# Kernel optimization log

Measured on AMD Instinct MI355X. Metric: run time of the kernel, lower is better.

## Reference

```python
import jax, jax.numpy as jnp
import numpy as np

N = 300000
H = 700
W_GRID = 700
CIN = 64
COUT = 64
K = 9


def setup_inputs() -> dict:
    rng = np.random.default_rng(0)
    lin = rng.permutation(H * W_GRID)[:N]
    ys = (lin // W_GRID).astype(np.int64)
    xs = (lin % W_GRID).astype(np.int64)
    grid = np.full(H * W_GRID, -1, np.int32)
    grid[lin] = np.arange(N, dtype=np.int32)
    offs = [(dy, dx) for dy in (-1, 0, 1) for dx in (-1, 0, 1)]

    def build(d):
        nbr = np.full((K, N), -1, np.int32)
        for k, (dy, dx) in enumerate(offs):
            ny = ys + dy * d
            nx = xs + dx * d
            valid = (ny >= 0) & (ny < H) & (nx >= 0) & (nx < W_GRID)
            l = np.clip(ny * W_GRID + nx, 0, H * W_GRID - 1)
            nbr[k] = np.where(valid, grid[l], -1)
        return jnp.asarray(nbr)

    nbr_d1 = build(1)
    nbr_d2 = build(2)

    key = jax.random.key(0)
    ks = jax.random.split(key, 16)
    f32 = jnp.float32

    def bn(k, c):
        s = jax.random.uniform(k, (c,), f32, 0.5, 1.5)
        b = jax.random.normal(jax.random.fold_in(k, 1), (c,), f32) * 0.1
        return s, b

    features = jax.random.normal(ks[0], (N, CIN), f32)
    W1 = jax.random.normal(ks[1], (K, CIN, COUT), f32) * 0.05
    W2a = jax.random.normal(ks[2], (CIN, COUT // 2), f32) * 0.05
    W2b = jax.random.normal(ks[3], (K, COUT // 2, COUT), f32) * 0.05
    W3 = jax.random.normal(ks[4], (K, CIN, COUT), f32) * 0.05
    Wf = jax.random.normal(ks[5], (3 * COUT, COUT), f32) * 0.05
    A1_w = jax.random.normal(ks[6], (3 * COUT, COUT // 4), f32) * 0.1
    A1_b = jnp.zeros((COUT // 4,), f32)
    A2_w = jax.random.normal(ks[7], (COUT // 4, 3 * COUT), f32) * 0.1
    A2_b = jnp.zeros((3 * COUT,), f32)
    bn1_s, bn1_b = bn(ks[8], COUT)
    bn2a_s, bn2a_b = bn(ks[9], COUT // 2)
    bn2b_s, bn2b_b = bn(ks[10], COUT)
    bn3_s, bn3_b = bn(ks[11], COUT)
    bnf_s, bnf_b = bn(ks[12], COUT)

    return dict(features=features, W1=W1, bn1_s=bn1_s, bn1_b=bn1_b,
                W2a=W2a, bn2a_s=bn2a_s, bn2a_b=bn2a_b,
                W2b=W2b, bn2b_s=bn2b_s, bn2b_b=bn2b_b,
                W3=W3, bn3_s=bn3_s, bn3_b=bn3_b,
                A1_w=A1_w, A1_b=A1_b, A2_w=A2_w, A2_b=A2_b,
                Wf=Wf, bnf_s=bnf_s, bnf_b=bnf_b,
                nbr_d1=nbr_d1, nbr_d2=nbr_d2)


def _sconv(f, nbr, W):
    # f: [N, Cin], nbr: [K, N] (-1 = no neighbor), W: [K, Cin, Cout]
    mask = (nbr >= 0)[..., None]                      # [K, N, 1]
    g = jnp.where(mask, f[jnp.clip(nbr, 0)], 0.0)     # [K, N, Cin] gather
    return jnp.einsum('knc,kcd->nd', g, W)            # [N, Cout]


def _bnrelu(x, s, b):
    # inference-mode BatchNorm folded into affine scale/shift, then ReLU
    return jax.nn.relu(x * s + b)


def reference(features, W1, bn1_s, bn1_b, W2a, bn2a_s, bn2a_b, W2b, bn2b_s, bn2b_b,
              W3, bn3_s, bn3_b, A1_w, A1_b, A2_w, A2_b, Wf, bnf_s, bnf_b,
              nbr_d1, nbr_d2):
    # path 1: 3x3 sparse conv + BN + ReLU
    feat1 = _bnrelu(_sconv(features, nbr_d1, W1), bn1_s, bn1_b)
    # path 2: 1x1 bottleneck + 3x3 sparse conv
    h = _bnrelu(features @ W2a, bn2a_s, bn2a_b)
    feat2 = _bnrelu(_sconv(h, nbr_d1, W2b), bn2b_s, bn2b_b)
    # path 3: 3x3 dilated (d=2) sparse conv
    feat3 = _bnrelu(_sconv(features, nbr_d2, W3), bn3_s, bn3_b)
    ms = jnp.concatenate([feat1, feat2, feat3], axis=1)   # [N, 3*Cout]
    # SE-style attention from global max pool over active sites
    pooled = jnp.max(ms, axis=0)                          # [3*Cout]
    attn = jax.nn.sigmoid(jax.nn.relu(pooled @ A1_w + A1_b) @ A2_w + A2_b)
    ms = ms * attn
    # 1x1 fusion conv + BN + ReLU
    fused = _bnrelu(ms @ Wf, bnf_s, bnf_b)                # [N, Cout]
    return fused
```

## Files before the change

### kernel.cpp

```cpp
#include <hip/hip_runtime.h>

#define N_PTS 300000
#define NPAD  300032
#define ZROW  N_PTS

typedef _Float16 f16;
typedef _Float16 f16x8 __attribute__((ext_vector_type(8)));
typedef float    f32x4 __attribute__((ext_vector_type(4)));

__device__ __forceinline__ f16 f2h(float x) { return (f16)x; }

union u4f16 { uint4 u; f16x8 h; };

#define HEAD_BLOCKS (NPAD / 256)
#define WP_BLOCKS   360


__global__ __launch_bounds__(256) void k_head(
    const float* __restrict__ feat, const float* __restrict__ W2a,
    const float* __restrict__ s2a, const float* __restrict__ b2a,
    const float* __restrict__ W1, const float* __restrict__ W2b,
    const float* __restrict__ W3,
    f16* __restrict__ featf, f16* __restrict__ hf,
    f16* __restrict__ Wt1, f16* __restrict__ Wt2b, f16* __restrict__ Wt3)
{
    if (blockIdx.x >= HEAD_BLOCKS) {
        int i = (blockIdx.x - HEAD_BLOCKS) * 256 + threadIdx.x;
        if (i < 36864) {
            int j = i & 7, lane = (i >> 3) & 63, nt = (i >> 9) & 3,
                ks = (i >> 11) & 1, k = i >> 12;
            int d = ks * 32 + (lane >> 4) * 8 + j, c = nt * 16 + (lane & 15);
            Wt1[i] = f2h(W1[(k << 12) + (d << 6) + c]);
        } else if (i < 73728) {
            int ii = i - 36864;
            int j = ii & 7, lane = (ii >> 3) & 63, nt = (ii >> 9) & 3,
                ks = (ii >> 11) & 1, k = ii >> 12;
            int d = ks * 32 + (lane >> 4) * 8 + j, c = nt * 16 + (lane & 15);
            Wt3[ii] = f2h(W3[(k << 12) + (d << 6) + c]);
        } else if (i < 92160) {
            int ii = i - 73728;
            int j = ii & 7, lane = (ii >> 3) & 63, nt = (ii >> 9) & 3, k = ii >> 11;
            int d = (lane >> 4) * 8 + j, c = nt * 16 + (lane & 15);
            Wt2b[ii] = f2h(W2b[k * 2048 + (d << 6) + c]);
        }
        return;
    }

    int lane = threadIdx.x & 63, wave = threadIdx.x >> 6;
    int n0 = (blockIdx.x * 4 + wave) * 64;
    int ln = lane & 15, q = lane >> 4;

    f16x8 a[4][2];
#pragma unroll
    for (int mt = 0; mt < 4; mt++) {
        int n = n0 + mt * 16 + ln;
#pragma unroll
        for (int ks = 0; ks < 2; ks++) {
            u4f16 v;
            if (n < N_PTS) {
                const float* p = feat + (long)n * 64 + ks * 32 + q * 8;
                float4 lo = *(const float4*)p;
                float4 hi = *(const float4*)(p + 4);
                v.h[0] = f2h(lo.x); v.h[1] = f2h(lo.y);
                v.h[2] = f2h(lo.z); v.h[3] = f2h(lo.w);
                v.h[4] = f2h(hi.x); v.h[5] = f2h(hi.y);
                v.h[6] = f2h(hi.z); v.h[7] = f2h(hi.w);
            } else {
                v.u = make_uint4(0u, 0u, 0u, 0u);
            }
            a[mt][ks] = v.h;
            *(uint4*)(featf + (long)n * 64 + ks * 32 + q * 8) = v.u;
        }
    }

    f32x4 acc[4][2];
    for (int mt = 0; mt < 4; mt++) for (int nt = 0; nt < 2; nt++)
        acc[mt][nt] = (f32x4){0.f, 0.f, 0.f, 0.f};
#pragma unroll
    for (int ks = 0; ks < 2; ks++)
#pragma unroll
        for (int nt = 0; nt < 2; nt++) {
            f16x8 b;
#pragma unroll
            for (int j = 0; j < 8; j++)
                b[j] = f2h(W2a[(ks * 32 + q * 8 + j) * 32 + nt * 16 + ln]);
#pragma unroll
            for (int mt = 0; mt < 4; mt++)
                acc[mt][nt] = __builtin_amdgcn_mfma_f32_16x16x32_f16(a[mt][ks], b, acc[mt][nt], 0, 0, 0);
        }

#pragma unroll
    for (int nt = 0; nt < 2; nt++) {
        int ch = nt * 16 + ln;
        float s = s2a[ch], bb = b2a[ch];
#pragma unroll
        for (int mt = 0; mt < 4; mt++)
#pragma unroll
            for (int r = 0; r < 4; r++) {
                int n = n0 + mt * 16 + q * 4 + r;
                float v = (n < N_PTS) ? fmaxf(acc[mt][nt][r] * s + bb, 0.f) : 0.f;
                hf[(long)n * 32 + ch] = f2h(v);
            }
    }
}

template <int CIN>
__device__ __forceinline__ void loadrows(
    uint4 (&dst)[4][CIN / 32], const int (&idx)[4],
    const f16* __restrict__ src, int q)
{
#pragma unroll
    for (int mt = 0; mt < 4; mt++) {
        const f16* p = src + (long)idx[mt] * CIN + q * 8;
#pragma unroll
        for (int ks = 0; ks < CIN / 32; ks++)
            dst[mt][ks] = *(const uint4*)(p + ks * 32);
    }
}

__device__ __forceinline__ void loadidx(
    int (&dst)[4], const int* __restrict__ nbr, int k, int n0, int ln)
{
    const int* nb = nbr + k * N_PTS;
#pragma unroll
    for (int mt = 0; mt < 4; mt++) {
        int nn = n0 + mt * 16 + ln;
        int v = (nn < N_PTS) ? nb[nn] : -1;
        dst[mt] = (v < 0) ? ZROW : v;
    }
}

template <int CIN>
__device__ __forceinline__ void conv_path(
    const f16* __restrict__ src, const f16* WtL,
    const int* __restrict__ nbr,
    int lane, int n0,
    const float* __restrict__ bns, const float* __restrict__ bnb,
    f16* __restrict__ msf, int colBase, float* __restrict__ pooled)
{
    constexpr int KS = CIN / 32;
    int ln = lane & 15, q = lane >> 4;

    f32x4 acc[4][4];
    for (int mt = 0; mt < 4; mt++) for (int nt = 0; nt < 4; nt++)
        acc[mt][nt] = (f32x4){0.f, 0.f, 0.f, 0.f};

    int  idxr[4][4];
    uint4 raw[4][4][KS];

#pragma unroll
    for (int k = 0; k < 4; k++) loadidx(idxr[k], nbr, k, n0, ln);
#pragma unroll
    for (int k = 0; k < 3; k++) loadrows<CIN>(raw[k], idxr[k], src, q);
    __builtin_amdgcn_sched_barrier(0);

#pragma unroll
    for (int k = 0; k < 9; k++) {
        if (k + 3 < 9) loadrows<CIN>(raw[(k + 3) & 3], idxr[(k + 3) & 3], src, q);
        if (k + 4 < 9) loadidx(idxr[k & 3], nbr, k + 4, n0, ln);
        __builtin_amdgcn_sched_barrier(0);
        const f16* Wk = WtL + k * (KS * 4 * 512);
        __builtin_amdgcn_s_setprio(1);
#pragma unroll
        for (int ks = 0; ks < KS; ks++)
#pragma unroll
            for (int nt = 0; nt < 4; nt++) {
                f16x8 b = *(const f16x8*)(Wk + (ks * 4 + nt) * 512 + lane * 8);
#pragma unroll
                for (int mt = 0; mt < 4; mt++) {
                    u4f16 v; v.u = raw[k & 3][mt][ks];
                    acc[mt][nt] = __builtin_amdgcn_mfma_f32_16x16x32_f16(v.h, b, acc[mt][nt], 0, 0, 0);
                }
            }
        __builtin_amdgcn_s_setprio(0);
    }

#pragma unroll
    for (int nt = 0; nt < 4; nt++) {
        int ch = colBase + nt * 16 + ln;
        float s = bns[nt * 16 + ln], bb = bnb[nt * 16 + ln];
        float cmax = 0.f;
#pragma unroll
        for (int mt = 0; mt < 4; mt++)
#pragma unroll
            for (int r = 0; r < 4; r++) {
                int n = n0 + mt * 16 + q * 4 + r;
                float v = fmaxf(acc[mt][nt][r] * s + bb, 0.f);
                msf[(long)n * 192 + ch] = f2h(v);
                if (n < N_PTS) cmax = fmaxf(cmax, v);
            }
        cmax = fmaxf(cmax, __shfl_xor(cmax, 16));
        cmax = fmaxf(cmax, __shfl_xor(cmax, 32));
        if (q == 0) atomicMax((int*)(pooled + ch), __float_as_int(cmax));
    }
}

__global__ __launch_bounds__(512, 2) void k_conv(
    const f16* __restrict__ featf, const f16* __restrict__ hf,
    const f16* __restrict__ Wt1, const f16* __restrict__ Wt2b, const f16* __restrict__ Wt3,
    const int* __restrict__ nbr1, const int* __restrict__ nbr2,
    const float* __restrict__ bn1_s, const float* __restrict__ bn1_b,
    const float* __restrict__ bn2b_s, const float* __restrict__ bn2b_b,
    const float* __restrict__ bn3_s, const float* __restrict__ bn3_b,
    f16* __restrict__ msf, float* __restrict__ pooled)
{
    __shared__ f16 smem[9 * 64 * 64];

    int path = blockIdx.x % 3;
    int g    = blockIdx.x / 3;
    int lane = threadIdx.x & 63, wave = threadIdx.x >> 6;
    int n0 = (g * 8 + wave) * 64;

    const f16* Wsrc = (path == 0) ? Wt1 : (path == 1) ? Wt2b : Wt3;
    int nchunk = (path == 1) ? (9 * 32 * 64 / 8) : (9 * 64 * 64 / 8);
    for (int i = threadIdx.x; i < nchunk; i += 512)
        ((uint4*)smem)[i] = ((const uint4*)Wsrc)[i];
    __syncthreads();

    if (path == 0)
        conv_path<64>(featf, smem, nbr1, lane, n0, bn1_s,  bn1_b,  msf, 0,   pooled);
    else if (path == 1)
        conv_path<32>(hf,    smem, nbr1, lane, n0, bn2b_s, bn2b_b, msf, 64,  pooled);
    else
        conv_path<64>(featf, smem, nbr2, lane, n0, bn3_s,  bn3_b,  msf, 128, pooled);
}

__global__ __launch_bounds__(256) void k_attn(
    const float* __restrict__ pooled,
    const float* __restrict__ A1w, const float* __restrict__ A1b,
    const float* __restrict__ A2w, const float* __restrict__ A2b,
    const float* __restrict__ Wf, f16* __restrict__ Wfst)
{
    __shared__ float sp[192], sa1[16], sattn[192];
    int t = threadIdx.x;
    if (t < 192) sp[t] = pooled[t];
    __syncthreads();
    if (t < 16) {
        float acc = A1b[t];
        for (int i = 0; i < 192; i++) acc += sp[i] * A1w[i * 16 + t];
        sa1[t] = fmaxf(acc, 0.f);
    }
    __syncthreads();
    if (t < 192) {
        float acc = A2b[t];
        for (int i = 0; i < 16; i++) acc += sa1[i] * A2w[i * 192 + t];
        sattn[t] = 1.f / (1.f + expf(-acc));
    }
    __syncthreads();
    for (int i = t; i < 12288; i += 256) {
        int j = i & 7, lane = (i >> 3) & 63, nt = (i >> 9) & 3, kt = i >> 11;
        int jrow = kt * 32 + (lane >> 4) * 8 + j, c = nt * 16 + (lane & 15);
        Wfst[i] = f2h(Wf[jrow * 64 + c] * sattn[jrow]);
    }
}

__global__ __launch_bounds__(256, 4) void k_fuse(
    const f16* __restrict__ msf, const f16* __restrict__ Wfst,
    const float* __restrict__ sf, const float* __restrict__ bf_,
    float* __restrict__ out)
{
    int lane = threadIdx.x & 63, wave = threadIdx.x >> 6;
    int n0 = (blockIdx.x * 4 + wave) * 32;
    int ln = lane & 15, q = lane >> 4;

    uint4 araw[6][2];
#pragma unroll
    for (int kt = 0; kt < 6; kt++)
#pragma unroll
        for (int mt = 0; mt < 2; mt++)
            araw[kt][mt] = *(const uint4*)(msf + (long)(n0 + mt * 16 + ln) * 192 + kt * 32 + q * 8);

    f32x4 acc[2][4];
    for (int mt = 0; mt < 2; mt++) for (int nt = 0; nt < 4; nt++)
        acc[mt][nt] = (f32x4){0.f, 0.f, 0.f, 0.f};

#pragma unroll
    for (int kt = 0; kt < 6; kt++)
#pragma unroll
        for (int nt = 0; nt < 4; nt++) {
            f16x8 b = *(const f16x8*)(Wfst + ((kt * 4 + nt) * 64 + lane) * 8);
#pragma unroll
            for (int mt = 0; mt < 2; mt++) {
                u4f16 v; v.u = araw[kt][mt];
                acc[mt][nt] = __builtin_amdgcn_mfma_f32_16x16x32_f16(v.h, b, acc[mt][nt], 0, 0, 0);
            }
        }

#pragma unroll
    for (int nt = 0; nt < 4; nt++) {
        int ch = nt * 16 + ln;
        float s = sf[ch], bb = bf_[ch];
#pragma unroll
        for (int mt = 0; mt < 2; mt++)
#pragma unroll
            for (int r = 0; r < 4; r++) {
                int n = n0 + mt * 16 + q * 4 + r;
                if (n < N_PTS)
                    out[(long)n * 64 + ch] = fmaxf(acc[mt][nt][r] * s + bb, 0.f);
            }
    }
}

extern "C" void kernel_launch(void* const* d_in, const int* in_sizes, int n_in,
                              void* d_out, int out_size, void* d_ws, size_t ws_size,
                              hipStream_t stream)
{
    const float* features = (const float*)d_in[0];
    const float* W1     = (const float*)d_in[1];
    const float* bn1_s  = (const float*)d_in[2];
    const float* bn1_b  = (const float*)d_in[3];
    const float* W2a    = (const float*)d_in[4];
    const float* bn2a_s = (const float*)d_in[5];
    const float* bn2a_b = (const float*)d_in[6];
    const float* W2b    = (const float*)d_in[7];
    const float* bn2b_s = (const float*)d_in[8];
    const float* bn2b_b = (const float*)d_in[9];
    const float* W3     = (const float*)d_in[10];
    const float* bn3_s  = (const float*)d_in[11];
    const float* bn3_b  = (const float*)d_in[12];
    const float* A1w    = (const float*)d_in[13];
    const float* A1b    = (const float*)d_in[14];
    const float* A2w    = (const float*)d_in[15];
    const float* A2b    = (const float*)d_in[16];
    const float* Wf     = (const float*)d_in[17];
    const float* bnf_s  = (const float*)d_in[18];
    const float* bnf_b  = (const float*)d_in[19];
    const int*   nbr1   = (const int*)d_in[20];
    const int*   nbr2   = (const int*)d_in[21];

    char* ws = (char*)d_ws;
    size_t off = 0;
    f16* featf = (f16*)(ws + off); off += (size_t)NPAD * 64 * 2;
    f16* hf    = (f16*)(ws + off); off += (size_t)NPAD * 32 * 2;
    f16* msf   = (f16*)(ws + off); off += (size_t)NPAD * 192 * 2;
    f16* Wt1   = (f16*)(ws + off); off += 9 * 64 * 64 * 2;
    f16* Wt3   = (f16*)(ws + off); off += 9 * 64 * 64 * 2;
    f16* Wt2b  = (f16*)(ws + off); off += 9 * 32 * 64 * 2;
    f16* Wfst  = (f16*)(ws + off); off += 192 * 64 * 2;
    float* pooled = (float*)(ws + off); off += 256 * 4;

    hipMemsetAsync(pooled, 0, 192 * sizeof(float), stream);

    k_head<<<HEAD_BLOCKS + WP_BLOCKS, 256, 0, stream>>>(
        features, W2a, bn2a_s, bn2a_b, W1, W2b, W3,
        featf, hf, Wt1, Wt2b, Wt3);
    k_conv<<<(NPAD / 64 / 8) * 3, 512, 0, stream>>>(featf, hf, Wt1, Wt2b, Wt3, nbr1, nbr2,
                                           bn1_s, bn1_b, bn2b_s, bn2b_b, bn3_s, bn3_b,
                                           msf, pooled);
    k_attn<<<1, 256, 0, stream>>>(pooled, A1w, A1b, A2w, A2b, Wf, Wfst);
    k_fuse<<<NPAD / 128, 256, 0, stream>>>(msf, Wfst, bnf_s, bnf_b, (float*)d_out);
}
```

Before: 419.6 us.

## Fuse attention into fusion kernel, halve conv weight LDS, use nontemporal stores

Removes the separate single-block attention kernel by having every fusion block recompute the SE attention and the attention-scaled fused weights into shared memory. The conv kernel now stages weights in two phases (first 4 taps, then 5) with an LDS footprint of 5 slices instead of 9, adding extra barriers mid-loop. Intermediate and output stores and the msf loads use nontemporal hints. The per-block recomputation of attention and weight transform adds redundant work to every fusion block in exchange for one fewer launch and dependency.

```diff
diff --git a/kernel.cpp b/kernel.cpp
--- a/kernel.cpp
+++ b/kernel.cpp
@@ -7,10 +7,11 @@
 typedef _Float16 f16;
 typedef _Float16 f16x8 __attribute__((ext_vector_type(8)));
 typedef float    f32x4 __attribute__((ext_vector_type(4)));
+typedef unsigned int u32x4 __attribute__((ext_vector_type(4)));
 
 __device__ __forceinline__ f16 f2h(float x) { return (f16)x; }
 
-union u4f16 { uint4 u; f16x8 h; };
+union u4f16 { uint4 u; u32x4 v; f16x8 h; };
 
 #define HEAD_BLOCKS (NPAD / 256)
 #define WP_BLOCKS   360
@@ -132,14 +133,19 @@
 
 template <int CIN>
 __device__ __forceinline__ void conv_path(
-    const f16* __restrict__ src, const f16* WtL,
+    const f16* __restrict__ src, f16* smem, const f16* __restrict__ Wsrc,
     const int* __restrict__ nbr,
-    int lane, int n0,
+    int lane, int n0, int tid,
     const float* __restrict__ bns, const float* __restrict__ bnb,
     f16* __restrict__ msf, int colBase, float* __restrict__ pooled)
 {
     constexpr int KS = CIN / 32;
+    constexpr int SLICE = CIN * 64;
     int ln = lane & 15, q = lane >> 4;
+
+    for (int i = tid; i < 4 * SLICE / 8; i += 512)
+        ((uint4*)smem)[i] = ((const uint4*)Wsrc)[i];
+    __syncthreads();
 
     f32x4 acc[4][4];
     for (int mt = 0; mt < 4; mt++) for (int nt = 0; nt < 4; nt++)
@@ -156,10 +162,16 @@
 
 #pragma unroll
     for (int k = 0; k < 9; k++) {
+        if (k == 4) {
+            __syncthreads();
+            for (int i = tid; i < 5 * SLICE / 8; i += 512)
+                ((uint4*)smem)[i] = ((const uint4*)(Wsrc + 4 * SLICE))[i];
+            __syncthreads();
+        }
         if (k + 3 < 9) loadrows<CIN>(raw[(k + 3) & 3], idxr[(k + 3) & 3], src, q);
         if (k + 4 < 9) loadidx(idxr[k & 3], nbr, k + 4, n0, ln);
         __builtin_amdgcn_sched_barrier(0);
-        const f16* Wk = WtL + k * (KS * 4 * 512);
+        const f16* Wk = smem + (k < 4 ? k : k - 4) * SLICE;
         __builtin_amdgcn_s_setprio(1);
 #pragma unroll
         for (int ks = 0; ks < KS; ks++)
@@ -186,7 +198,7 @@
             for (int r = 0; r < 4; r++) {
                 int n = n0 + mt * 16 + q * 4 + r;
                 float v = fmaxf(acc[mt][nt][r] * s + bb, 0.f);
-                msf[(long)n * 192 + ch] = f2h(v);
+                __builtin_nontemporal_store(f2h(v), &msf[(long)n * 192 + ch]);
                 if (n < N_PTS) cmax = fmaxf(cmax, v);
             }
         cmax = fmaxf(cmax, __shfl_xor(cmax, 16));
@@ -204,71 +216,65 @@
     const float* __restrict__ bn3_s, const float* __restrict__ bn3_b,
     f16* __restrict__ msf, float* __restrict__ pooled)
 {
-    __shared__ f16 smem[9 * 64 * 64];
+    __shared__ f16 smem[5 * 64 * 64];
 
     int path = blockIdx.x % 3;
     int g    = blockIdx.x / 3;
     int lane = threadIdx.x & 63, wave = threadIdx.x >> 6;
     int n0 = (g * 8 + wave) * 64;
-
-    const f16* Wsrc = (path == 0) ? Wt1 : (path == 1) ? Wt2b : Wt3;
-    int nchunk = (path == 1) ? (9 * 32 * 64 / 8) : (9 * 64 * 64 / 8);
-    for (int i = threadIdx.x; i < nchunk; i += 512)
-        ((uint4*)smem)[i] = ((const uint4*)Wsrc)[i];
-    __syncthreads();
+    int tid = threadIdx.x;
 
     if (path == 0)
-        conv_path<64>(featf, smem, nbr1, lane, n0, bn1_s,  bn1_b,  msf, 0,   pooled);
+        conv_path<64>(featf, smem, Wt1,  nbr1, lane, n0, tid, bn1_s,  bn1_b,  msf, 0,   pooled);
     else if (path == 1)
-        conv_path<32>(hf,    smem, nbr1, lane, n0, bn2b_s, bn2b_b, msf, 64,  pooled);
+        conv_path<32>(hf,    smem, Wt2b, nbr1, lane, n0, tid, bn2b_s, bn2b_b, msf, 64,  pooled);
     else
-        conv_path<64>(featf, smem, nbr2, lane, n0, bn3_s,  bn3_b,  msf, 128, pooled);
-}
-
-__global__ __launch_bounds__(256) void k_attn(
-    const float* __restrict__ pooled,
+        conv_path<64>(featf, smem, Wt3,  nbr2, lane, n0, tid, bn3_s,  bn3_b,  msf, 128, pooled);
+}
+
+__global__ __launch_bounds__(256, 4) void k_fuse(
+    const f16* __restrict__ msf, const float* __restrict__ pooled,
     const float* __restrict__ A1w, const float* __restrict__ A1b,
     const float* __restrict__ A2w, const float* __restrict__ A2b,
-    const float* __restrict__ Wf, f16* __restrict__ Wfst)
+    const float* __restrict__ Wf,
+    const float* __restrict__ sf, const float* __restrict__ bf_,
+    float* __restrict__ out)
 {
     __shared__ float sp[192], sa1[16], sattn[192];
+    __shared__ f16 sWf[12288];
     int t = threadIdx.x;
     if (t < 192) sp[t] = pooled[t];
     __syncthreads();
     if (t < 16) {
-        float acc = A1b[t];
-        for (int i = 0; i < 192; i++) acc += sp[i] * A1w[i * 16 + t];
-        sa1[t] = fmaxf(acc, 0.f);
+        float a = A1b[t];
+        for (int i = 0; i < 192; i++) a += sp[i] * A1w[i * 16 + t];
+        sa1[t] = fmaxf(a, 0.f);
     }
     __syncthreads();
     if (t < 192) {
-        float acc = A2b[t];
-        for (int i = 0; i < 16; i++) acc += sa1[i] * A2w[i * 192 + t];
-        sattn[t] = 1.f / (1.f + expf(-acc));
+        float a = A2b[t];
+        for (int i = 0; i < 16; i++) a += sa1[i] * A2w[i * 192 + t];
+        sattn[t] = 1.f / (1.f + expf(-a));
     }
     __syncthreads();
     for (int i = t; i < 12288; i += 256) {
         int j = i & 7, lane = (i >> 3) & 63, nt = (i >> 9) & 3, kt = i >> 11;
         int jrow = kt * 32 + (lane >> 4) * 8 + j, c = nt * 16 + (lane & 15);
-        Wfst[i] = f2h(Wf[jrow * 64 + c] * sattn[jrow]);
-    }
-}
-
-__global__ __launch_bounds__(256, 4) void k_fuse(
-    const f16* __restrict__ msf, const f16* __restrict__ Wfst,
-    const float* __restrict__ sf, const float* __restrict__ bf_,
-    float* __restrict__ out)
-{
+        sWf[i] = f2h(Wf[jrow * 64 + c] * sattn[jrow]);
+    }
+    __syncthreads();
+
     int lane = threadIdx.x & 63, wave = threadIdx.x >> 6;
     int n0 = (blockIdx.x * 4 + wave) * 32;
     int ln = lane & 15, q = lane >> 4;
 
-    uint4 araw[6][2];
+    u32x4 araw[6][2];
 #pragma unroll
     for (int kt = 0; kt < 6; kt++)
 #pragma unroll
         for (int mt = 0; mt < 2; mt++)
-            araw[kt][mt] = *(const uint4*)(msf + (long)(n0 + mt * 16 + ln) * 192 + kt * 32 + q * 8);
+            araw[kt][mt] = __builtin_nontemporal_load(
+                (const u32x4*)(msf + (long)(n0 + mt * 16 + ln) * 192 + kt * 32 + q * 8));
 
     f32x4 acc[2][4];
     for (int mt = 0; mt < 2; mt++) for (int nt = 0; nt < 4; nt++)
@@ -278,10 +284,10 @@
     for (int kt = 0; kt < 6; kt++)
 #pragma unroll
         for (int nt = 0; nt < 4; nt++) {
-            f16x8 b = *(const f16x8*)(Wfst + ((kt * 4 + nt) * 64 + lane) * 8);
+            f16x8 b = *(const f16x8*)(sWf + ((kt * 4 + nt) * 64 + lane) * 8);
 #pragma unroll
             for (int mt = 0; mt < 2; mt++) {
-                u4f16 v; v.u = araw[kt][mt];
+                u4f16 v; v.v = araw[kt][mt];
                 acc[mt][nt] = __builtin_amdgcn_mfma_f32_16x16x32_f16(v.h, b, acc[mt][nt], 0, 0, 0);
             }
         }
@@ -296,7 +302,8 @@
             for (int r = 0; r < 4; r++) {
                 int n = n0 + mt * 16 + q * 4 + r;
                 if (n < N_PTS)
-                    out[(long)n * 64 + ch] = fmaxf(acc[mt][nt][r] * s + bb, 0.f);
+                    __builtin_nontemporal_store(fmaxf(acc[mt][nt][r] * s + bb, 0.f),
+                                                &out[(long)n * 64 + ch]);
             }
     }
 }
@@ -338,6 +345,7 @@
     f16* Wt2b  = (f16*)(ws + off); off += 9 * 32 * 64 * 2;
     f16* Wfst  = (f16*)(ws + off); off += 192 * 64 * 2;
     float* pooled = (float*)(ws + off); off += 256 * 4;
+    (void)Wfst;
 
     hipMemsetAsync(pooled, 0, 192 * sizeof(float), stream);
 
@@ -347,6 +355,6 @@
     k_conv<<<(NPAD / 64 / 8) * 3, 512, 0, stream>>>(featf, hf, Wt1, Wt2b, Wt3, nbr1, nbr2,
                                            bn1_s, bn1_b, bn2b_s, bn2b_b, bn3_s, bn3_b,
                                            msf, pooled);
-    k_attn<<<1, 256, 0, stream>>>(pooled, A1w, A1b, A2w, A2b, Wf, Wfst);
-    k_fuse<<<NPAD / 128, 256, 0, stream>>>(msf, Wfst, bnf_s, bnf_b, (float*)d_out);
-}
+    k_fuse<<<NPAD / 128, 256, 0, stream>>>(msf, pooled, A1w, A1b, A2w, A2b, Wf,
+                                           bnf_s, bnf_b, (float*)d_out);
+}
```

Result: slower. 457.6 us (+9.0%).
